# Kernel tuning notes

Measured on AMD Instinct MI355X. Metric: run time of the kernel, lower is better.

## Reference

```python
import jax, jax.numpy as jnp
import numpy as np

BIG = 1e9      # infinity sentinel used by the CUDA kernels
THRESH = 1e8   # 'min_val >= 1e8 -> invalid' cutoff
MAX_LEN = 512  # init kwarg max_length
BANDWIDTH = 0.2


def _dist(X, Y):
    # pairwise squared-euclidean: D[b,i,j] = sum_d (X[b,i,d]-Y[b,j,d])^2
    diff = X[:, :, None, :] - Y[:, None, :, :]  # [B,N,M,d]
    return jnp.sum(diff * diff, axis=-1)        # [B,N,M]


def _ldtw_dp(D, max_len, bandwidth):
    """Band-limited length-constrained DTW DP.
    Returns (min_vals[B], choices[max_len,B,N,M] int8, best_k[B]).
    choices[t] holds the step-(k=t+1) decisions at interior cells (i-1, j-1)."""
    B, N, M = D.shape
    ii = np.arange(1, N + 1)[:, None]
    jj = np.arange(1, M + 1)[None, :]
    band_bad = jnp.asarray((np.abs(ii - jj) > bandwidth * max(N, M)) & (bandwidth > 0))  # [N,M] static

    # prev_cost padded [B, N+2, M+2]; only (0,0) starts at 0, everything else BIG.
    prev0 = jnp.full((B, N + 2, M + 2), BIG, jnp.float32).at[:, 0, 0].set(0.0)

    def step(prev, _):
        # candidates for interior cells (i in 1..N, j in 1..M)
        cand = jnp.stack(
            [prev[:, 0:N, 0:M],       # diag  (choice 0)
             prev[:, 0:N, 1:M + 1],   # vert  (choice 1)
             prev[:, 1:N + 1, 0:M]],  # hori  (choice 2)
            axis=0)                    # [3,B,N,M]
        min_val = cand.min(axis=0)
        # argmin returns first minimum -> matches strict-less update order (diag,vert,hori)
        choice = jnp.argmin(cand, axis=0).astype(jnp.int8)
        valid = min_val < THRESH
        cost = jnp.where(band_bad[None] | ~valid, BIG, min_val + D)
        ch = jnp.where(valid & ~band_bad[None], choice, jnp.int8(-1))
        curr = jnp.full_like(prev, BIG).at[:, 1:N + 1, 1:M + 1].set(cost)
        return curr, (cost[:, N - 1, M - 1], ch)

    _, (final_costs, choices) = jax.lax.scan(step, prev0, None, length=max_len)
    # final_costs[t] is the cost of a length-(t+1) path ending at (N,M)
    mvl = max(N, M)
    valid_costs = final_costs[mvl - 1:]            # k in [mvl, max_len]
    min_vals = valid_costs.min(axis=0)             # [B]
    best_k = jnp.argmin(valid_costs, axis=0) + mvl # [B] (unused in fwd)
    return min_vals, choices, best_k


def setup_inputs() -> dict:
    key = jax.random.key(0)
    k1, k2 = jax.random.split(key)
    X = jax.random.normal(k1, (16, 256, 64), jnp.float32)
    Y = jax.random.normal(k2, (16, 256, 64), jnp.float32)
    return {"X": X, "Y": Y}


def reference(X, Y):
    D = _dist(X, Y)
    min_vals, _, _ = _ldtw_dp(D, MAX_LEN, BANDWIDTH)
    # original module returns (min_vals, None); the None carries no information
    return min_vals
```

## Files before the change

### kernel.cpp

```cpp
#include <hip/hip_runtime.h>

#define BIGV 1e9f
#define NPT 256

__device__ __forceinline__ int imin_of(int s){
    int a = s - 255; if (a < 0) a = 0;
    int c = s - 50;  c = (c > 0) ? (c >> 1) : 0;
    return (a > c) ? a : c;
}
__device__ __forceinline__ int imax_of(int s){
    int a = (s < 255) ? s : 255;
    int c = (s + 51) >> 1;
    return (a < c) ? a : c;
}

__device__ __forceinline__ float dpp_shr1(float x){
    return __int_as_float(__builtin_amdgcn_update_dpp(
        __float_as_int(BIGV), __float_as_int(x), 0x138 , 0xF, 0xF, false));
}
__device__ __forceinline__ float dpp_shl1(float x){
    return __int_as_float(__builtin_amdgcn_update_dpp(
        __float_as_int(BIGV), __float_as_int(x), 0x130 , 0xF, 0xF, false));
}

__device__ __forceinline__ float min3f(float a, float b, float c){
    float r;
    asm("v_min3_f32 %0, %1, %2, %3" : "=v"(r) : "v"(a), "v"(b), "v"(c));
    return r;
}

__global__ __launch_bounds__(256) void ldtw_dist(const float* __restrict__ X,
                                                 const float* __restrict__ Y,
                                                 float* __restrict__ Df)
{
    __shared__ float4 Xs[96*17];
    __shared__ float4 Ys[96*17];
    __shared__ float nX[96], nY[96];
    __shared__ float Band[64*65];
    const int b  = blockIdx.x >> 3;
    const int c  = blockIdx.x & 7;
    const int s0 = c << 6;
    const int s1 = (s0 + 63 > 510) ? 510 : (s0 + 63);
    const int ilo = imin_of(s0), ihi = imax_of(s1);
    const int jlo = s0 - imax_of(s0), jhi = s1 - imin_of(s1);
    const int nx = ihi - ilo + 1, ny = jhi - jlo + 1;
    const int t = threadIdx.x;
    const float4* Xb = (const float4*)(X + (size_t)b * NPT * 64);
    const float4* Yb = (const float4*)(Y + (size_t)b * NPT * 64);

    for (int idx = t; idx < nx * 16; idx += 256){
        int r = idx >> 4, k = idx & 15;
        Xs[r*17 + k] = Xb[(ilo + r)*16 + k];
    }
    for (int idx = t; idx < ny * 16; idx += 256){
        int r = idx >> 4, k = idx & 15;
        Ys[r*17 + k] = Yb[(jlo + r)*16 + k];
    }
    __syncthreads();

    for (int r = t; r < nx + ny; r += 256){
        const float4* row = (r < nx) ? (Xs + r*17) : (Ys + (r - nx)*17);
        float acc = 0.f;
        #pragma unroll
        for (int k = 0; k < 16; ++k){
            float4 v = row[k];
            acc += v.x*v.x + v.y*v.y + v.z*v.z + v.w*v.w;
        }
        if (r < nx) nX[r] = acc; else nY[r - nx] = acc;
    }
    __syncthreads();

    for (int slot = t; slot < 64*64; slot += 256){
        const int l  = slot >> 6;
        const int sd = slot & 63;
        const int s  = s0 + sd;
        if (s > 510) continue;
        const int im = imin_of(s);
        const int i  = im + l;
        if (i > imax_of(s)) continue;
        const int j  = s - i;
        const float4* xr = Xs + (i - ilo)*17;
        const float4* yr = Ys + (j - jlo)*17;
        float dot = 0.f;
        #pragma unroll
        for (int k = 0; k < 16; ++k){
            float4 a = xr[k], bb = yr[k];
            dot += a.x*bb.x + a.y*bb.y + a.z*bb.z + a.w*bb.w;
        }
        Band[sd*65 + l] = nX[i - ilo] + nY[j - jlo] - 2.f*dot;
    }
    __syncthreads();

    float4* Df4 = (float4*)Df;
    const size_t rowbase4 = ((size_t)(b * 512 + s0)) << 6;
    for (int slot = t; slot < 64*64; slot += 256){
        const int sd = slot >> 6, q = slot & 63;
        const int s  = s0 + sd;
        float4 v = make_float4(BIGV, BIGV, BIGV, BIGV);
        if (s <= 510){
            const int im = imin_of(s), ix = imax_of(s);
            const int i0 = q << 2;
            if (i0 + 0 >= im && i0 + 0 <= ix) v.x = Band[sd*65 + (i0 + 0 - im)];
            if (i0 + 1 >= im && i0 + 1 <= ix) v.y = Band[sd*65 + (i0 + 1 - im)];
            if (i0 + 2 >= im && i0 + 2 <= ix) v.z = Band[sd*65 + (i0 + 2 - im)];
            if (i0 + 3 >= im && i0 + 3 <= ix) v.w = Band[sd*65 + (i0 + 3 - im)];
        }
        Df4[rowbase4 + ((size_t)sd << 6) + q] = v;
    }
}

__global__ __launch_bounds__(64) void ldtw_dp(const float* __restrict__ Df,
                                              float* __restrict__ out)
{
    const int b = blockIdx.x;
    const int L = threadIdx.x;
    const float4* base = (const float4*)Df + ((size_t)b << 15) + L;

    float p0, p1, p2, p3, q0, q1, q2, q3;
    float d00 = Df[(size_t)b << 17];
    p0 = (L == 0) ? d00 : BIGV; p1 = BIGV; p2 = BIGV; p3 = BIGV;
    q0 = BIGV; q1 = BIGV; q2 = BIGV; q3 = BIGV;

#define LOADG(Bk, g) { \
    const float4* r0_ = base + (size_t)(((g) << 3) + 1) * 64; \
    const float4* r1_ = r0_ + 256; \
    Bk##0 = r0_[0];   Bk##1 = r0_[64];  Bk##2 = r0_[128]; Bk##3 = r0_[192]; \
    Bk##4 = r1_[0];   Bk##5 = r1_[64];  Bk##6 = r1_[128]; Bk##7 = r1_[192]; }

#define STEP_PQ(V) { \
    float s1_ = dpp_shr1(p3), s2_ = dpp_shr1(q3); \
    float n0 = min3f(s1_, p0, s2_) + (V).x; \
    float n1 = min3f(p0, p1, q0) + (V).y; \
    float n2 = min3f(p1, p2, q1) + (V).z; \
    float n3 = min3f(p2, p3, q2) + (V).w; \
    q0 = n0; q1 = n1; q2 = n2; q3 = n3; }
#define STEP_QP(V) { \
    float s1_ = dpp_shr1(q3), s2_ = dpp_shr1(p3); \
    float n0 = min3f(s1_, q0, s2_) + (V).x; \
    float n1 = min3f(q0, q1, p0) + (V).y; \
    float n2 = min3f(q1, q2, p1) + (V).z; \
    float n3 = min3f(q2, q3, p2) + (V).w; \
    p0 = n0; p1 = n1; p2 = n2; p3 = n3; }

#define GROUP8(Bk) \
    STEP_PQ(Bk##0) STEP_QP(Bk##1) STEP_PQ(Bk##2) STEP_QP(Bk##3) \
    STEP_PQ(Bk##4) STEP_QP(Bk##5) STEP_PQ(Bk##6) STEP_QP(Bk##7)

    float4 A0,A1,A2,A3,A4,A5,A6,A7;
    float4 B0,B1,B2,B3,B4,B5,B6,B7;
    float4 C0,C1,C2,C3,C4,C5,C6,C7;
    float4 E0,E1,E2,E3,E4,E5,E6,E7;
    LOADG(A, 0) LOADG(B, 1) LOADG(C, 2) LOADG(E, 3)
    for (int m = 0; m < 60; m += 4){
        GROUP8(A) LOADG(A, m + 4)
        GROUP8(B) LOADG(B, m + 5)
        GROUP8(C) LOADG(C, m + 6)
        GROUP8(E) LOADG(E, m + 7)
    }
    GROUP8(A)
    GROUP8(B)
    GROUP8(C)
    STEP_PQ(E0) STEP_QP(E1) STEP_PQ(E2) STEP_QP(E3) STEP_PQ(E4) STEP_QP(E5)

    if (L == 63) out[b] = p3;
#undef LOADG
#undef STEP_PQ
#undef STEP_QP
#undef GROUP8
}

__device__ __forceinline__ float cell_d(const float4* __restrict__ Xb,
                                        const float4* __restrict__ Yb,
                                        int i, int j)
{
    const float4* xr = Xb + i*16;
    const float4* yr = Yb + j*16;
    float acc = 0.f;
    #pragma unroll
    for (int k = 0; k < 16; ++k){
        float4 a = xr[k], bb = yr[k];
        float dx = a.x-bb.x, dy = a.y-bb.y, dz = a.z-bb.z, dw = a.w-bb.w;
        acc += dx*dx + dy*dy + dz*dz + dw*dw;
    }
    return acc;
}

__global__ __launch_bounds__(64) void ldtw_fused_fb(const float* __restrict__ X,
                                                    const float* __restrict__ Y,
                                                    float* __restrict__ out)
{
    const int b = blockIdx.x;
    const int l = threadIdx.x;
    const float4* Xb = (const float4*)(X + (size_t)b * NPT * 64);
    const float4* Yb = (const float4*)(Y + (size_t)b * NPT * 64);
    float prev1 = (l == 0) ? cell_d(Xb, Yb, 0, 0) : BIGV;
    float prev2 = BIGV;
    int base1 = 0, base2 = 0;
    for (int s = 1; s <= 510; ++s){
        const int im = imin_of(s);
        const int ix = imax_of(s);
        const int i  = im + l;
        const bool act = (i <= ix);
        const int ic = act ? i : ix;
        const int j  = s - ic;
        float Dv = cell_d(Xb, Yb, ic, j);
        const int d1 = im - base1, d2 = im - base2;
        float sr1 = dpp_shr1(prev1), sl1 = dpp_shl1(prev1);
        float sr2 = dpp_shr1(prev2), sl2 = dpp_shl1(prev2);
        float m1 = d1 ? fminf(prev1, sl1) : fminf(sr1, prev1);
        float vd = (d2 == 0) ? sr2 : ((d2 == 2) ? sl2 : prev2);
        float m3 = fminf(m1, vd);
        float cur = act ? (m3 + Dv) : BIGV;
        prev2 = prev1; base2 = base1;
        prev1 = cur;   base1 = im;
    }
    if (l == 0) out[b] = prev1;
}

extern "C" void kernel_launch(void* const* d_in, const int* in_sizes, int n_in,
                              void* d_out, int out_size, void* d_ws, size_t ws_size,
                              hipStream_t stream)
{
    const float* X = (const float*)d_in[0];
    const float* Y = (const float*)d_in[1];
    float* out = (float*)d_out;
    const int Bn = in_sizes[0] / (NPT * 64);
    const size_t need = (size_t)Bn * 512 * 256 * 4 + 4096;
    if (ws_size >= need){
        float* Df = (float*)d_ws;
        hipLaunchKernelGGL(ldtw_dist, dim3(Bn * 8), dim3(256), 0, stream, X, Y, Df);
        hipLaunchKernelGGL(ldtw_dp,   dim3(Bn),     dim3(64),  0, stream, Df, out);
    } else {
        hipLaunchKernelGGL(ldtw_fused_fb, dim3(Bn), dim3(64), 0, stream, X, Y, out);
    }
}
```

Before: 37.83 us.

## Register-tile band distance as 6x6 outer product and deepen DP prefetch

The distance kernel now has each thread compute a 6x6 block of dot products over the full 96x96 X/Y tile held in shared memory. Each loaded float4 is reused across six partial products, replacing per-cell dot products that reloaded both rows. Only cells inside the current diagonal band are written back. The DP kernel's prefetch ring grows from four to six groups of distance rows, with the group index clamped, to hide more global load latency behind the serial wavefront. The costs are redundant work on off-band cells, much higher register pressure in both kernels, and a slightly larger workspace requirement.

```diff
diff --git a/kernel.cpp b/kernel.cpp
--- a/kernel.cpp
+++ b/kernel.cpp
@@ -70,24 +70,46 @@
     }
     __syncthreads();
 
-    for (int slot = t; slot < 64*64; slot += 256){
-        const int l  = slot >> 6;
-        const int sd = slot & 63;
-        const int s  = s0 + sd;
-        if (s > 510) continue;
-        const int im = imin_of(s);
-        const int i  = im + l;
-        if (i > imax_of(s)) continue;
-        const int j  = s - i;
-        const float4* xr = Xs + (i - ilo)*17;
-        const float4* yr = Ys + (j - jlo)*17;
-        float dot = 0.f;
+    {
+        const int ti = t >> 4;
+        const int tj = t & 15;
+        float acc[6][6];
+        #pragma unroll
+        for (int u = 0; u < 6; ++u)
+            #pragma unroll
+            for (int v = 0; v < 6; ++v) acc[u][v] = 0.f;
+
         #pragma unroll
         for (int k = 0; k < 16; ++k){
-            float4 a = xr[k], bb = yr[k];
-            dot += a.x*bb.x + a.y*bb.y + a.z*bb.z + a.w*bb.w;
-        }
-        Band[sd*65 + l] = nX[i - ilo] + nY[j - jlo] - 2.f*dot;
+            float4 xa[6], ya[6];
+            #pragma unroll
+            for (int u = 0; u < 6; ++u){
+                xa[u] = Xs[(ti + u*16)*17 + k];
+                ya[u] = Ys[(tj + u*16)*17 + k];
+            }
+            #pragma unroll
+            for (int u = 0; u < 6; ++u)
+                #pragma unroll
+                for (int v = 0; v < 6; ++v)
+                    acc[u][v] += xa[u].x*ya[v].x + xa[u].y*ya[v].y
+                               + xa[u].z*ya[v].z + xa[u].w*ya[v].w;
+        }
+
+        #pragma unroll
+        for (int u = 0; u < 6; ++u){
+            #pragma unroll
+            for (int v = 0; v < 6; ++v){
+                const int iloc = ti + u*16, jloc = tj + v*16;
+                const int i = ilo + iloc, j = jlo + jloc;
+                const int s = i + j;
+                if (s >= s0 && s <= s1){
+                    const int im = imin_of(s), ix = imax_of(s);
+                    if (i >= im && i <= ix)
+                        Band[(s - s0)*65 + (i - im)] =
+                            nX[iloc] + nY[jloc] - 2.f*acc[u][v];
+                }
+            }
+        }
     }
     __syncthreads();
 
@@ -122,7 +144,8 @@
     q0 = BIGV; q1 = BIGV; q2 = BIGV; q3 = BIGV;
 
 #define LOADG(Bk, g) { \
-    const float4* r0_ = base + (size_t)(((g) << 3) + 1) * 64; \
+    const int gg_ = ((g) > 63) ? 63 : (g); \
+    const float4* r0_ = base + (size_t)((gg_ << 3) + 1) * 64; \
     const float4* r1_ = r0_ + 256; \
     Bk##0 = r0_[0];   Bk##1 = r0_[64];  Bk##2 = r0_[128]; Bk##3 = r0_[192]; \
     Bk##4 = r1_[0];   Bk##5 = r1_[64];  Bk##6 = r1_[128]; Bk##7 = r1_[192]; }
@@ -150,12 +173,16 @@
     float4 B0,B1,B2,B3,B4,B5,B6,B7;
     float4 C0,C1,C2,C3,C4,C5,C6,C7;
     float4 E0,E1,E2,E3,E4,E5,E6,E7;
-    LOADG(A, 0) LOADG(B, 1) LOADG(C, 2) LOADG(E, 3)
-    for (int m = 0; m < 60; m += 4){
-        GROUP8(A) LOADG(A, m + 4)
-        GROUP8(B) LOADG(B, m + 5)
-        GROUP8(C) LOADG(C, m + 6)
-        GROUP8(E) LOADG(E, m + 7)
+    float4 F0,F1,F2,F3,F4,F5,F6,F7;
+    float4 G0,G1,G2,G3,G4,G5,G6,G7;
+    LOADG(A, 0) LOADG(B, 1) LOADG(C, 2) LOADG(E, 3) LOADG(F, 4) LOADG(G, 5)
+    for (int m = 0; m < 60; m += 6){
+        GROUP8(A) LOADG(A, m + 6)
+        GROUP8(B) LOADG(B, m + 7)
+        GROUP8(C) LOADG(C, m + 8)
+        GROUP8(E) LOADG(E, m + 9)
+        GROUP8(F) LOADG(F, m + 10)
+        GROUP8(G) LOADG(G, m + 11)
     }
     GROUP8(A)
     GROUP8(B)
@@ -225,7 +252,7 @@
     const float* Y = (const float*)d_in[1];
     float* out = (float*)d_out;
     const int Bn = in_sizes[0] / (NPT * 64);
-    const size_t need = (size_t)Bn * 512 * 256 * 4 + 4096;
+    const size_t need = (size_t)Bn * 512 * 256 * 4 + 65536;
     if (ws_size >= need){
         float* Df = (float*)d_ws;
         hipLaunchKernelGGL(ldtw_dist, dim3(Bn * 8), dim3(256), 0, stream, X, Y, Df);
```

After: 110.0 us. 191% more time.
